# Performance work log

Hardware: AMD Instinct MI355X
Metric: run time of the kernel (lower is better)

Reference implementation:

```python
import jax, jax.numpy as jnp
import numpy as np

ALPHA = 0.3

def setup_inputs() -> dict:
    key = jax.random.key(0)
    k1, k2, k3, k4 = jax.random.split(key, 4)
    bz, sl, n_pos = 64, 1024, 50
    a_arc = jax.random.normal(k1, (bz, sl, sl), dtype=jnp.float32)
    s_arc = jax.random.normal(k2, (bz, sl, sl), dtype=jnp.float32)
    adds = jax.random.randint(k3, (bz, sl), 0, n_pos, dtype=jnp.int32)
    pos = jax.random.randint(k4, (bz, sl), 0, n_pos, dtype=jnp.int32)
    return {"a_arc": a_arc, "s_arc": s_arc, "adds": adds, "pos": pos, "n_pos": n_pos}


def reference(a_arc, s_arc, adds, pos, n_pos):
    # Bin index for every (head, dep) pair: bin = adds[b,i]*n_pos + adds[b,j]
    bins_add = adds[:, :, None] * n_pos + adds[:, None, :]          # [bz, sl, sl] int32
    # Histogram: sum a_arc values per POS-pair bin (replaces the O(n_pos^2) masked loop)
    score_arc = jax.ops.segment_sum(
        a_arc.reshape(-1), bins_add.reshape(-1), num_segments=n_pos * n_pos)
    score_arc = jax.nn.sigmoid(score_arc)                            # [n_pos^2]
    # Broadcast the binned scores back onto s_arc via the pos-pair bins
    bins_pos = pos[:, :, None] * n_pos + pos[:, None, :]             # [bz, sl, sl]
    return s_arc + ALPHA * score_arc[bins_pos]
```

## Files before the change

### kernel.cpp

```cpp
#include <hip/hip_runtime.h>

constexpr int NPOS  = 50;
constexpr int NBINS = NPOS * NPOS;
constexpr int SL    = 1024;
constexpr int BZ    = 64;
constexpr float ALPHA = 0.3f;

using nat_f4 = __attribute__((ext_vector_type(4))) float;

constexpr int NRNG      = 8;
constexpr int NHALF     = 2;
constexpr int PSLICE    = 352;
constexpr int H_THREADS = 256;
constexpr int H_BLOCKS  = BZ * NRNG * NHALF;

__device__ __forceinline__ int rng_lo(int r) { return r < 2 ? 7 * r : 14 + 6 * (r - 2); }
__device__ __forceinline__ int rng_sz(int r) { return r < 2 ? 7 : 6; }

constexpr int R2_THREADS = 256;
constexpr int R2_BLOCKS  = (NBINS + R2_THREADS - 1) / R2_THREADS;
constexpr int A_THREADS      = 256;
constexpr int ROWS_PER_BLOCK = 32;
constexpr int BLOCKS_PER_B   = SL / ROWS_PER_BLOCK;
constexpr int A_BLOCKS       = BZ * BLOCKS_PER_B;

__global__ __launch_bounds__(H_THREADS) void hist_gather(
    const float* __restrict__ a, const int* __restrict__ adds,
    float* __restrict__ g_part) {
  __shared__ int   adds_s[SL];
  __shared__ float accL[8][SL];
  __shared__ int   list[512 + 8];
  __shared__ int   order2[SL];
  __shared__ int   cnt8[8], off8[8];
  __shared__ int   cntQ[NPOS], offQs[NPOS], offQm[NPOS];
  __shared__ int   nrows_s;

  const int tid  = threadIdx.x;
  const int b    = blockIdx.x / (NRNG * NHALF);
  const int rem  = blockIdx.x % (NRNG * NHALF);
  const int rg   = rem >> 1;
  const int half = rem & 1;
  const int lo   = rng_lo(rg), sz = rng_sz(rg);
  const int rlo  = half * (SL / NHALF), rhi = rlo + SL / NHALF;

  ((int4*)adds_s)[tid] = ((const int4*)(adds + (size_t)b * SL))[tid];
  #pragma unroll
  for (int p = 0; p < 8; ++p) ((float4*)&accL[p][0])[tid] = float4{0, 0, 0, 0};
  if (tid < 8) cnt8[tid] = 0;
  if (tid < NPOS) cntQ[tid] = 0;
  __syncthreads();

  for (int i = tid; i < SL; i += H_THREADS) atomicAdd(&cntQ[adds_s[i]], 1);
  for (int i = rlo + tid; i < rhi; i += H_THREADS) {
    const int pl = adds_s[i] - lo;
    if ((unsigned)pl < (unsigned)sz) atomicAdd(&cnt8[pl], 1);
  }
  __syncthreads();
  if (tid == 0) {
    int run = 0;
    #pragma unroll
    for (int c = 0; c < 8; ++c) { off8[c] = run; run += cnt8[c]; }
    nrows_s = run;
  } else if (tid == 64) {
    int run = 0;
    for (int c = 0; c < NPOS; ++c) { offQs[c] = run; offQm[c] = run; run += cntQ[c]; }
  }
  __syncthreads();
  for (int i = rlo + tid; i < rhi; i += H_THREADS) {
    const int pl = adds_s[i] - lo;
    if ((unsigned)pl < (unsigned)sz)
      list[atomicAdd(&off8[pl], 1)] = (pl << 12) | i;
  }
  for (int i = tid; i < SL; i += H_THREADS)
    order2[atomicAdd(&offQm[adds_s[i]], 1)] = i;
  __syncthreads();
  const int N    = nrows_s;
  const int Npad = (N + 7) & ~7;
  if (tid < 8 && N + tid < Npad)
    list[N + tid] = (7 << 12) | (N > 0 ? (list[N - 1] & 0xFFF) : 0);
  __syncthreads();

  const nat_f4* __restrict__ Ab = (const nat_f4*)(a + (size_t)b * SL * SL);
  float4 creg = {0, 0, 0, 0};
  int pcur = 7;

  int    eA[8], eB[8];
  nat_f4 vA[8], vB[8];
  auto loadbank = [&](int (&e)[8], nat_f4 (&v)[8], int k) {
    #pragma unroll
    for (int u = 0; u < 8; ++u) {
      e[u] = __builtin_amdgcn_readfirstlane(list[k + u]);
      v[u] = __builtin_nontemporal_load(
          Ab + (size_t)(e[u] & 0xFFF) * (SL / 4) + tid);
    }
  };
  auto procbank = [&](int (&e)[8], nat_f4 (&v)[8]) {
    #pragma unroll
    for (int u = 0; u < 8; ++u) {
      const int pl = e[u] >> 12;
      if (pl != pcur) {
        ((float4*)&accL[pcur][0])[tid] = creg;
        creg = float4{0, 0, 0, 0};
        pcur = pl;
      }
      creg.x += v[u][0]; creg.y += v[u][1]; creg.z += v[u][2]; creg.w += v[u][3];
    }
  };

  if (Npad > 0) {
    pcur = list[0] >> 12;
    loadbank(eA, vA, 0);
    for (int k = 0; k < Npad; k += 16) {
      if (k + 8 < Npad) loadbank(eB, vB, k + 8);
      procbank(eA, vA);
      if (k + 16 < Npad) loadbank(eA, vA, k + 16);
      if (k + 8 < Npad) procbank(eB, vB);
    }
    ((float4*)&accL[pcur][0])[tid] = creg;
  }
  __syncthreads();

  float* __restrict__ gp = g_part + (size_t)blockIdx.x * PSLICE;
  for (int bin = tid; bin < sz * NPOS; bin += H_THREADS) {
    const int pl = bin / NPOS, q = bin % NPOS;
    const int s0 = offQs[q], n = cntQ[q];
    float s = 0.0f;
    for (int k2 = 0; k2 < n; ++k2) s += accL[pl][order2[s0 + k2]];
    gp[bin] = s;
  }
}

__global__ __launch_bounds__(R2_THREADS) void reduce2(
    const float* __restrict__ g_part, float* __restrict__ g_hist) {
  const int bin = blockIdx.x * R2_THREADS + threadIdx.x;
  if (bin >= NBINS) return;
  const int p = bin / NPOS, q = bin % NPOS;
  const int rg = (p < 14) ? p / 7 : 2 + (p - 14) / 6;
  const int pl = (p < 14) ? p % 7 : (p - 14) % 6;
  const float* __restrict__ base =
      g_part + (size_t)(rg * NHALF) * PSLICE + pl * NPOS + q;
  float s = 0.0f;
  #pragma unroll 8
  for (int bb = 0; bb < BZ; ++bb) {
    const size_t o = (size_t)bb * (NRNG * NHALF) * PSLICE;
    s += base[o] + base[o + PSLICE];
  }
  g_hist[bin] = s;
}

__global__ __launch_bounds__(A_THREADS) void apply_kernel(
    const float* __restrict__ s, const int* __restrict__ pos,
    const float* __restrict__ g_hist, float* __restrict__ out) {
  __shared__ float sig[NBINS];
  __shared__ int   pos_s[SL];

  const int tid = threadIdx.x;
  const int b   = blockIdx.x / BLOCKS_PER_B;
  const int i0  = (blockIdx.x % BLOCKS_PER_B) * ROWS_PER_BLOCK;

  ((int4*)pos_s)[tid] = ((const int4*)(pos + (size_t)b * SL))[tid];
  for (int k = tid; k < NBINS; k += A_THREADS) {
    const float h = g_hist[k];
    sig[k] = 1.0f / (1.0f + __expf(-h));
  }
  __syncthreads();

  const int4 pj = ((const int4*)pos_s)[tid];
  const size_t rowoff = ((size_t)b * SL + i0) * SL;
  const nat_f4* __restrict__ srow = (const nat_f4*)(s + rowoff);
  nat_f4* __restrict__ orow = (nat_f4*)(out + rowoff);

  for (int r = 0; r < ROWS_PER_BLOCK; ++r) {
    const int base = pos_s[i0 + r] * NPOS;
    const nat_f4 sv =
        __builtin_nontemporal_load(srow + (size_t)r * (SL / 4) + tid);
    nat_f4 ov;
    ov[0] = sv[0] + ALPHA * sig[base + pj.x];
    ov[1] = sv[1] + ALPHA * sig[base + pj.y];
    ov[2] = sv[2] + ALPHA * sig[base + pj.z];
    ov[3] = sv[3] + ALPHA * sig[base + pj.w];
    __builtin_nontemporal_store(ov, orow + (size_t)r * (SL / 4) + tid);
  }
}

extern "C" void kernel_launch(void* const* d_in, const int* in_sizes, int n_in,
                              void* d_out, int out_size, void* d_ws, size_t ws_size,
                              hipStream_t stream) {
  const float* a_arc = (const float*)d_in[0];
  const float* s_arc = (const float*)d_in[1];
  const int*   adds  = (const int*)d_in[2];
  const int*   pos   = (const int*)d_in[3];
  float* out    = (float*)d_out;
  float* g_hist = (float*)d_ws;
  float* g_part = g_hist + 4096;

  hist_gather <<<H_BLOCKS, H_THREADS, 0, stream>>>(a_arc, adds, g_part);
  reduce2     <<<R2_BLOCKS, R2_THREADS, 0, stream>>>(g_part, g_hist);
  apply_kernel<<<A_BLOCKS, A_THREADS, 0, stream>>>(s_arc, pos, g_hist, out);
}
```

Baseline: 159.5 us.

## Precompute per-batch sort metadata in a setup kernel shared by histogram blocks

```diff
diff --git a/kernel.cpp b/kernel.cpp
--- a/kernel.cpp
+++ b/kernel.cpp
@@ -11,11 +11,14 @@
 constexpr int NRNG      = 8;
 constexpr int NHALF     = 2;
 constexpr int PSLICE    = 352;
+constexpr int LISTCAP   = 520;
 constexpr int H_THREADS = 256;
 constexpr int H_BLOCKS  = BZ * NRNG * NHALF;
 
 __device__ __forceinline__ int rng_lo(int r) { return r < 2 ? 7 * r : 14 + 6 * (r - 2); }
 __device__ __forceinline__ int rng_sz(int r) { return r < 2 ? 7 : 6; }
+
+constexpr int META_STRIDE = 4096;
 
 constexpr int R2_THREADS = 256;
 constexpr int R2_BLOCKS  = (NBINS + R2_THREADS - 1) / R2_THREADS;
@@ -24,16 +27,57 @@
 constexpr int BLOCKS_PER_B   = SL / ROWS_PER_BLOCK;
 constexpr int A_BLOCKS       = BZ * BLOCKS_PER_B;
 
+__global__ __launch_bounds__(256) void setup_kernel(
+    const int* __restrict__ adds, int* __restrict__ g_meta) {
+  __shared__ int adds_s[SL];
+  __shared__ int cntQ[NPOS], offQ[NPOS], offQm[NPOS];
+  __shared__ int cntP[2][NPOS], offP[2][NPOS], offPm[2][NPOS];
+
+  const int tid = threadIdx.x, b = blockIdx.x;
+  ((int4*)adds_s)[tid] = ((const int4*)(adds + (size_t)b * SL))[tid];
+  if (tid < NPOS) { cntQ[tid] = 0; cntP[0][tid] = 0; cntP[1][tid] = 0; }
+  __syncthreads();
+
+  for (int i = tid; i < SL; i += 256) {
+    const int p = adds_s[i];
+    atomicAdd(&cntQ[p], 1);
+    atomicAdd(&cntP[i >> 9][p], 1);
+  }
+  __syncthreads();
+  if (tid == 0) {
+    int run = 0;
+    for (int c = 0; c < NPOS; ++c) { offQ[c] = run; offQm[c] = run; run += cntQ[c]; }
+  } else if (tid == 64) {
+    int run = 0;
+    for (int c = 0; c < NPOS; ++c) { offP[0][c] = run; offPm[0][c] = run; run += cntP[0][c]; }
+  } else if (tid == 128) {
+    int run = 0;
+    for (int c = 0; c < NPOS; ++c) { offP[1][c] = run; offPm[1][c] = run; run += cntP[1][c]; }
+  }
+  __syncthreads();
+
+  int* __restrict__ gm = g_meta + (size_t)b * META_STRIDE;
+  for (int i = tid; i < SL; i += 256) {
+    const int p = adds_s[i], h = i >> 9;
+    gm[atomicAdd(&offQm[p], 1)] = i;
+    gm[2048 + h * 512 + atomicAdd(&offPm[h][p], 1)] = (p << 12) | i;
+  }
+  if (tid < NPOS) {
+    gm[1024 + tid] = cntQ[tid];
+    gm[1074 + tid] = offQ[tid];
+    gm[1124 + tid] = offP[0][tid];
+    gm[1175 + tid] = offP[1][tid];
+  }
+  if (tid == 0) { gm[1124 + 50] = 512; gm[1175 + 50] = 512; }
+}
+
 __global__ __launch_bounds__(H_THREADS) void hist_gather(
-    const float* __restrict__ a, const int* __restrict__ adds,
+    const float* __restrict__ a, const int* __restrict__ g_meta,
     float* __restrict__ g_part) {
-  __shared__ int   adds_s[SL];
   __shared__ float accL[8][SL];
-  __shared__ int   list[512 + 8];
+  __shared__ int   list[LISTCAP];
   __shared__ int   order2[SL];
-  __shared__ int   cnt8[8], off8[8];
-  __shared__ int   cntQ[NPOS], offQs[NPOS], offQm[NPOS];
-  __shared__ int   nrows_s;
+  __shared__ int   cntQ[NPOS], offQs[NPOS];
 
   const int tid  = threadIdx.x;
   const int b    = blockIdx.x / (NRNG * NHALF);
@@ -41,40 +85,19 @@
   const int rg   = rem >> 1;
   const int half = rem & 1;
   const int lo   = rng_lo(rg), sz = rng_sz(rg);
-  const int rlo  = half * (SL / NHALF), rhi = rlo + SL / NHALF;
-
-  ((int4*)adds_s)[tid] = ((const int4*)(adds + (size_t)b * SL))[tid];
+
+  const int* __restrict__ gm = g_meta + (size_t)b * META_STRIDE;
+  const int s0 = gm[1124 + half * 51 + lo];
+  const int s1 = gm[1124 + half * 51 + lo + sz];
+  const int N  = s1 - s0;
+
+  ((int4*)order2)[tid] = ((const int4*)gm)[tid];
+  if (tid < NPOS) { cntQ[tid] = gm[1024 + tid]; offQs[tid] = gm[1074 + tid]; }
+  for (int i = tid; i < N; i += H_THREADS)
+    list[i] = gm[2048 + half * 512 + s0 + i] - (lo << 12);
   #pragma unroll
   for (int p = 0; p < 8; ++p) ((float4*)&accL[p][0])[tid] = float4{0, 0, 0, 0};
-  if (tid < 8) cnt8[tid] = 0;
-  if (tid < NPOS) cntQ[tid] = 0;
-  __syncthreads();
-
-  for (int i = tid; i < SL; i += H_THREADS) atomicAdd(&cntQ[adds_s[i]], 1);
-  for (int i = rlo + tid; i < rhi; i += H_THREADS) {
-    const int pl = adds_s[i] - lo;
-    if ((unsigned)pl < (unsigned)sz) atomicAdd(&cnt8[pl], 1);
-  }
-  __syncthreads();
-  if (tid == 0) {
-    int run = 0;
-    #pragma unroll
-    for (int c = 0; c < 8; ++c) { off8[c] = run; run += cnt8[c]; }
-    nrows_s = run;
-  } else if (tid == 64) {
-    int run = 0;
-    for (int c = 0; c < NPOS; ++c) { offQs[c] = run; offQm[c] = run; run += cntQ[c]; }
-  }
-  __syncthreads();
-  for (int i = rlo + tid; i < rhi; i += H_THREADS) {
-    const int pl = adds_s[i] - lo;
-    if ((unsigned)pl < (unsigned)sz)
-      list[atomicAdd(&off8[pl], 1)] = (pl << 12) | i;
-  }
-  for (int i = tid; i < SL; i += H_THREADS)
-    order2[atomicAdd(&offQm[adds_s[i]], 1)] = i;
-  __syncthreads();
-  const int N    = nrows_s;
+  __syncthreads();
   const int Npad = (N + 7) & ~7;
   if (tid < 8 && N + tid < Npad)
     list[N + tid] = (7 << 12) | (N > 0 ? (list[N - 1] & 0xFFF) : 0);
@@ -123,9 +146,9 @@
   float* __restrict__ gp = g_part + (size_t)blockIdx.x * PSLICE;
   for (int bin = tid; bin < sz * NPOS; bin += H_THREADS) {
     const int pl = bin / NPOS, q = bin % NPOS;
-    const int s0 = offQs[q], n = cntQ[q];
+    const int q0 = offQs[q], n = cntQ[q];
     float s = 0.0f;
-    for (int k2 = 0; k2 < n; ++k2) s += accL[pl][order2[s0 + k2]];
+    for (int k2 = 0; k2 < n; ++k2) s += accL[pl][order2[q0 + k2]];
     gp[bin] = s;
   }
 }
@@ -192,9 +215,11 @@
   const int*   pos   = (const int*)d_in[3];
   float* out    = (float*)d_out;
   float* g_hist = (float*)d_ws;
-  float* g_part = g_hist + 4096;
-
-  hist_gather <<<H_BLOCKS, H_THREADS, 0, stream>>>(a_arc, adds, g_part);
+  int*   g_meta = (int*)(g_hist + 4096);
+  float* g_part = (float*)(g_meta + BZ * META_STRIDE);
+
+  setup_kernel<<<BZ, 256, 0, stream>>>(adds, g_meta);
+  hist_gather <<<H_BLOCKS, H_THREADS, 0, stream>>>(a_arc, g_meta, g_part);
   reduce2     <<<R2_BLOCKS, R2_THREADS, 0, stream>>>(g_part, g_hist);
   apply_kernel<<<A_BLOCKS, A_THREADS, 0, stream>>>(s_arc, pos, g_hist, out);
 }
```

Result: no change. 160.2 us (+0.5%).
